# Kernel optimization log

Measured on AMD Instinct MI355X. Metric: run time of the kernel, lower is better.

Reference implementation:

```python
import jax, jax.numpy as jnp
import numpy as np
import math

B, S, HID = 16, 512, 768
NUM_LABELS = 9
NUM_HEADS = 4
HEAD_DIM = HID // NUM_HEADS
MAX_REL = 5
B_PERSON = 1
I_PERSON = 2
LN_EPS = 1e-5


def setup_inputs() -> dict:
    key = jax.random.key(0)
    ks = jax.random.split(key, 16)
    w = lambda k, shp: jax.random.normal(k, shp, dtype=jnp.float32) * 0.02
    return {
        "sequence_output": jax.random.normal(ks[0], (B, S, HID), dtype=jnp.float32),
        "Wq": w(ks[1], (HID, HID)), "bq": jnp.zeros((HID,), jnp.float32),
        "Wk": w(ks[2], (HID, HID)), "bk": jnp.zeros((HID,), jnp.float32),
        "Wv": w(ks[3], (HID, HID)), "bv": jnp.zeros((HID,), jnp.float32),
        "Wo": w(ks[4], (HID, HID)), "bo": jnp.zeros((HID,), jnp.float32),
        "ln_g": jnp.ones((HID,), jnp.float32), "ln_b": jnp.zeros((HID,), jnp.float32),
        "Ws": w(ks[5], (HID, NUM_LABELS)), "bs": jnp.zeros((NUM_LABELS,), jnp.float32),
        "entity_bias": w(ks[6], (NUM_LABELS,)),
    }


def _heads(x):
    # [B,S,HID] -> [B,H,S,D]
    return x.reshape(B, S, NUM_HEADS, HEAD_DIM).transpose(0, 2, 1, 3)


def reference(sequence_output, Wq, bq, Wk, bk, Wv, bv, Wo, bo, ln_g, ln_b, Ws, bs, entity_bias):
    x = sequence_output
    q = _heads(x @ Wq + bq)
    k = _heads(x @ Wk + bk)
    v = _heads(x @ Wv + bv)

    scores = jnp.einsum("bhqd,bhkd->bhqk", q, k)
    # relative position bias: exp(-0.1 * clamp(|i-j|, 0, MAX_REL)), broadcast over b,h
    idx = jnp.arange(S, dtype=jnp.float32)
    dist = jnp.abs(idx[None, :] - idx[:, None])  # [S,S]
    rel_bias = jnp.exp(-0.1 * jnp.clip(dist, 0.0, float(MAX_REL)))
    dist_mask = -0.1 * dist
    scores = (scores + rel_bias) / math.sqrt(HEAD_DIM) + dist_mask
    probs = jax.nn.softmax(scores, axis=-1)  # dropout is identity in eval

    ctx = jnp.einsum("bhqk,bhkd->bhqd", probs, v)
    ctx = ctx.transpose(0, 2, 1, 3).reshape(B, S, HID)
    out = ctx @ Wo + bo

    h = x + out
    mu = jnp.mean(h, axis=-1, keepdims=True)
    var = jnp.mean(jnp.square(h - mu), axis=-1, keepdims=True)
    h = (h - mu) * jax.lax.rsqrt(var + LN_EPS) * ln_g + ln_b

    span_logits = h @ Ws + bs  # [B,S,L]
    # vectorized entity-bias post-process: the torch loop adds entity_bias[I_PERSON]
    # TWICE to final_logits[:, j, I_PERSON] whenever argmax(span_logits[:, j-1]) == B_PERSON
    prev_is_b = jnp.argmax(span_logits[:, :-1], axis=-1) == B_PERSON  # [B,S-1]
    bump = jnp.where(prev_is_b, 2.0 * entity_bias[I_PERSON], 0.0)
    final_logits = span_logits.at[:, 1:, I_PERSON].add(bump)
    return final_logits
```

## Files before the change

kernel.cpp:

```cpp
#include <hip/hip_runtime.h>
#include <math.h>

#define SEQ 512
#define HID 768
#define NBATCH 16
#define ROWS 8192
#define INV_SQRT_D 0.07216878364870323f

typedef short s8v __attribute__((ext_vector_type(8)));
typedef _Float16 h8v __attribute__((ext_vector_type(8)));
typedef float f4v __attribute__((ext_vector_type(4)));
typedef unsigned short u16;

__device__ __forceinline__ u16 f2h(float f) {
  _Float16 h = (_Float16)f;
  return __builtin_bit_cast(u16, h);
}

template <int KSTEPS>
__device__ __forceinline__ void mm_core128(
    const u16* __restrict__ A, const int lda,
    const u16* __restrict__ B, const int ldb,
    u16* lds, f4v (&acc)[4][4])
{
  const int tid = threadIdx.x;
  const int w = tid >> 6, ln = tid & 63;
  const u16* src = (w >> 1) ? B : A;
  const int ld = (w >> 1) ? ldb : lda;
  const int half = w & 1;
  const int srow = ln >> 2;
  const int csw  = ((ln & 3) - (ln >> 3)) & 3;
  const int ml = ln & 15, quad = ln >> 4;
  const int fo2 = ((quad + ((ln >> 1) & 3)) & 3) * 8;
  const int wr = (w >> 1) * 64, wc = (w & 1) * 64;

  const u16* gp[4];
  int lpo[4];
#pragma unroll
  for (int t = 0; t < 4; ++t) {
    const int row = half * 64 + t * 16 + srow;
    gp[t]  = src + (size_t)row * ld + csw * 8;
    lpo[t] = (w >> 1) * 4096 + half * 2048 + t * 512 + ln * 8;
  }
  s8v c[8];
#pragma unroll
  for (int t = 0; t < 4; ++t) {
    c[t]     = *(const s8v*)gp[t];
    c[4 + t] = *(const s8v*)(gp[t] + 32);
  }

  for (int kp = 0; kp < KSTEPS / 2; ++kp) {
    __syncthreads();
#pragma unroll
    for (int t = 0; t < 4; ++t) {
      *(s8v*)&lds[lpo[t]]        = c[t];
      *(s8v*)&lds[8192 + lpo[t]] = c[4 + t];
    }
    __syncthreads();
    if (kp + 1 < KSTEPS / 2) {
      const int k0 = (kp + 1) * 64;
#pragma unroll
      for (int t = 0; t < 4; ++t) {
        c[t]     = *(const s8v*)(gp[t] + k0);
        c[4 + t] = *(const s8v*)(gp[t] + k0 + 32);
      }
    }
#pragma unroll
    for (int sub = 0; sub < 2; ++sub) {
      const int so = sub * 8192;
      h8v a[4], b[4];
#pragma unroll
      for (int i = 0; i < 4; ++i)
        a[i] = *(const h8v*)&lds[so + (wr + i * 16 + ml) * 32 + fo2];
#pragma unroll
      for (int j = 0; j < 4; ++j)
        b[j] = *(const h8v*)&lds[so + 4096 + (wc + j * 16 + ml) * 32 + fo2];
#pragma unroll
      for (int i = 0; i < 4; ++i)
#pragma unroll
        for (int j = 0; j < 4; ++j)
          acc[i][j] = __builtin_amdgcn_mfma_f32_16x16x32_f16(a[i], b[j], acc[i][j], 0, 0, 0);
    }
  }
}

__global__ __launch_bounds__(256) void splitx(const float* __restrict__ x,
                                              u16* __restrict__ xh)
{
  const int i = blockIdx.x * 256 + threadIdx.x;
  const float4 v = ((const float4*)x)[i];
  ((ushort4*)xh)[i] = make_ushort4(f2h(v.x), f2h(v.y), f2h(v.z), f2h(v.w));
}

__global__ __launch_bounds__(256) void wsplit(
    const float* __restrict__ Wq, const float* __restrict__ Wk,
    const float* __restrict__ Wv, const float* __restrict__ Wo,
    u16* __restrict__ WTh)
{
  __shared__ float t[32][33];
  const int z = blockIdx.z;
  const float* W = (z == 0) ? Wq : (z == 1) ? Wk : (z == 2) ? Wv : Wo;
  const int n0 = blockIdx.x * 32, k0 = blockIdx.y * 32;
  const int tx = threadIdx.x & 31, ty = threadIdx.x >> 5;
#pragma unroll
  for (int i = 0; i < 4; ++i)
    t[ty + 8 * i][tx] = W[(size_t)(k0 + ty + 8 * i) * HID + n0 + tx];
  __syncthreads();
#pragma unroll
  for (int i = 0; i < 4; ++i) {
    const float v = t[tx][ty + 8 * i];
    const size_t idx = (size_t)z * HID * HID + (size_t)(n0 + ty + 8 * i) * HID + k0 + tx;
    WTh[idx] = f2h(v);
  }
}

__global__ __launch_bounds__(256, 3) void qkv_mm(
    const u16* __restrict__ xh, const u16* __restrict__ WTh,
    const float* __restrict__ bq, const float* __restrict__ bk, const float* __restrict__ bv,
    u16* __restrict__ qh, u16* __restrict__ kh, u16* __restrict__ vtmp16)
{
  __shared__ u16 lds[16384];
  const int id = blockIdx.x;
  const int xcd = id & 7;
  const int s = id >> 3;
  const int bx = s % 6;
  const int yl = (s / 6) & 7;
  const int z  = s / 48;
  const int bm = (yl * 8 + xcd) * 128;
  const int bn = bx * 128;
  const size_t wtoff = (size_t)z * HID * HID + (size_t)bn * HID;
  f4v acc[4][4];
#pragma unroll
  for (int i = 0; i < 4; ++i)
#pragma unroll
    for (int j = 0; j < 4; ++j) acc[i][j] = (f4v)0.f;
  mm_core128<24>(xh + (size_t)bm * HID, HID, WTh + wtoff, HID, lds, acc);
  const int tid = threadIdx.x, w = tid >> 6, ln = tid & 63;
  const int ml = ln & 15, quad = ln >> 4;
  const int wr = (w >> 1) * 64, wc = (w & 1) * 64;
  const float* bias = (z == 0) ? bq : (z == 1) ? bk : bv;
#pragma unroll
  for (int i = 0; i < 4; ++i)
#pragma unroll
    for (int j = 0; j < 4; ++j) {
      const int gcol = bn + wc + j * 16 + ml;
      const float bv_ = bias[gcol];
#pragma unroll
      for (int r = 0; r < 4; ++r) {
        const int grow = bm + wr + i * 16 + quad * 4 + r;
        const float v = acc[i][j][r] + bv_;
        const size_t idx = (size_t)grow * HID + gcol;
        if (z == 2)      vtmp16[idx] = f2h(v);
        else if (z == 0) qh[idx] = f2h(v);
        else             kh[idx] = f2h(v);
      }
    }
}

__global__ __launch_bounds__(256) void vtrans(const u16* __restrict__ vtmp16,
                                              u16* __restrict__ vTh)
{
  __shared__ u16 t[32][33];
  const int b = blockIdx.z, n0 = blockIdx.x * 32, c0 = blockIdx.y * 32;
  const int tx = threadIdx.x & 31, ty = threadIdx.x >> 5;
  const u16* src = vtmp16 + (size_t)b * SEQ * HID;
#pragma unroll
  for (int i = 0; i < 4; ++i)
    t[ty + 8 * i][tx] = src[(size_t)(c0 + ty + 8 * i) * HID + n0 + tx];
  __syncthreads();
#pragma unroll
  for (int i = 0; i < 4; ++i) {
    const size_t idx = (size_t)b * HID * SEQ + (size_t)(n0 + ty + 8 * i) * SEQ + c0 + tx;
    vTh[idx] = t[tx][ty + 8 * i];
  }
}

__global__ __launch_bounds__(256, 2) void attn_fused(
    const u16* __restrict__ qh, const u16* __restrict__ kh,
    const u16* __restrict__ vTh, u16* __restrict__ ch)
{
  __shared__ u16 lds[28928];
  __shared__ float gtab[1024];
  __shared__ float red[4][32];
  const int f = blockIdx.x;
  const int xcd = f & 7, s = f >> 3;
  const int z = xcd * 8 + (s >> 4);
  const int bm = (s & 15) * 32;
  const int b = z >> 2, hh = z & 3;
  const int tid = threadIdx.x, w = tid >> 6, ln = tid & 63;
  const int ml = ln & 15, quad = ln >> 4;

  for (int t = tid; t < 1023; t += 256) {
    const float fd = fabsf((float)(t - 511));
    gtab[t] = INV_SQRT_D * __expf(-0.1f * fminf(fd, 5.0f)) - 0.1f * fd;
  }

  const u16* qbase = qh + (size_t)(b * SEQ + bm) * HID + hh * 192;
  const u16* kbase = kh + (size_t)b * SEQ * HID + hh * 192;
  const u16* vbase = vTh + (size_t)b * HID * SEQ + (size_t)(hh * 192) * SEQ;

  h8v qf[2][6];
#pragma unroll
  for (int i = 0; i < 2; ++i)
#pragma unroll
    for (int ks = 0; ks < 6; ++ks)
      qf[i][ks] = *(const h8v*)(qbase + (size_t)(i * 16 + ml) * HID + ks * 32 + quad * 8);

  int koff[6], kldso[6], voff[6], vldso[6];
#pragma unroll
  for (int c = 0; c < 6; ++c) {
    const int cc = c * 256 + tid;
    const int krow = cc / 24, kcol = cc % 24;
    koff[c]  = krow * HID + kcol * 8;
    kldso[c] = krow * 200 + kcol * 8;
    const int vrow = cc >> 3, vcol = cc & 7;
    voff[c]  = vrow * SEQ + vcol * 8;
    vldso[c] = 12800 + vrow * 72 + vcol * 8;
  }
  s8v kc[6], vc[6];
#pragma unroll
  for (int c = 0; c < 6; ++c) {
    kc[c] = *(const s8v*)(kbase + koff[c]);
    vc[c] = *(const s8v*)(vbase + voff[c]);
  }

  f4v acc2[2][3];
#pragma unroll
  for (int i = 0; i < 2; ++i)
#pragma unroll
    for (int jj = 0; jj < 3; ++jj) acc2[i][jj] = (f4v)0.f;
  float rsum[2][4];
#pragma unroll
  for (int i = 0; i < 2; ++i)
#pragma unroll
    for (int r = 0; r < 4; ++r) rsum[i][r] = 0.f;

  for (int j = 0; j < 8; ++j) {
    __syncthreads();
#pragma unroll
    for (int c = 0; c < 6; ++c) {
      *(s8v*)&lds[kldso[c]] = kc[c];
      *(s8v*)&lds[vldso[c]] = vc[c];
    }
    __syncthreads();
    if (j < 7) {
      const int ko = (j + 1) * 64;
#pragma unroll
      for (int c = 0; c < 6; ++c) {
        kc[c] = *(const s8v*)(kbase + (size_t)ko * HID + koff[c]);
        vc[c] = *(const s8v*)(vbase + ko + voff[c]);
      }
    }
    f4v sacc[2];
    sacc[0] = (f4v)0.f; sacc[1] = (f4v)0.f;
    __builtin_amdgcn_s_setprio(1);
#pragma unroll
    for (int ks = 0; ks < 6; ++ks) {
      const h8v kf = *(const h8v*)&lds[(w * 16 + ml) * 200 + ks * 32 + quad * 8];
      sacc[0] = __builtin_amdgcn_mfma_f32_16x16x32_f16(qf[0][ks], kf, sacc[0], 0, 0, 0);
      sacc[1] = __builtin_amdgcn_mfma_f32_16x16x32_f16(qf[1][ks], kf, sacc[1], 0, 0, 0);
    }
    __builtin_amdgcn_s_setprio(0);
    const int scolg = j * 64 + w * 16 + ml;
#pragma unroll
    for (int i = 0; i < 2; ++i)
#pragma unroll
      for (int r = 0; r < 4; ++r) {
        const int lrow = i * 16 + quad * 4 + r;
        const float g = gtab[bm + lrow - scolg + 511];
        const float p = __expf(fmaf(sacc[i][r], INV_SQRT_D, g));
        rsum[i][r] += p;
        lds[26624 + lrow * 72 + w * 16 + ml] = f2h(p);
      }
    __syncthreads();
    __builtin_amdgcn_s_setprio(1);
#pragma unroll
    for (int ks = 0; ks < 2; ++ks) {
      h8v pf[2], vf[3];
#pragma unroll
      for (int i = 0; i < 2; ++i)
        pf[i] = *(const h8v*)&lds[26624 + (i * 16 + ml) * 72 + ks * 32 + quad * 8];
#pragma unroll
      for (int jj = 0; jj < 3; ++jj)
        vf[jj] = *(const h8v*)&lds[12800 + (w * 48 + jj * 16 + ml) * 72 + ks * 32 + quad * 8];
#pragma unroll
      for (int i = 0; i < 2; ++i)
#pragma unroll
        for (int jj = 0; jj < 3; ++jj)
          acc2[i][jj] = __builtin_amdgcn_mfma_f32_16x16x32_f16(pf[i], vf[jj], acc2[i][jj], 0, 0, 0);
    }
    __builtin_amdgcn_s_setprio(0);
  }

#pragma unroll
  for (int i = 0; i < 2; ++i)
#pragma unroll
    for (int r = 0; r < 4; ++r) {
      float t = rsum[i][r];
#pragma unroll
      for (int o = 1; o < 16; o <<= 1) t += __shfl_xor(t, o, 64);
      rsum[i][r] = t;
    }
  if (ml == 0) {
#pragma unroll
    for (int i = 0; i < 2; ++i)
#pragma unroll
      for (int r = 0; r < 4; ++r) red[w][i * 16 + quad * 4 + r] = rsum[i][r];
  }
  __syncthreads();

#pragma unroll
  for (int i = 0; i < 2; ++i)
#pragma unroll
    for (int r = 0; r < 4; ++r) {
      const int R = i * 16 + quad * 4 + r;
      const float is = 1.0f / (red[0][R] + red[1][R] + red[2][R] + red[3][R]);
      const int m = bm + R;
#pragma unroll
      for (int jj = 0; jj < 3; ++jj) {
        const int gcol = hh * 192 + w * 48 + jj * 16 + ml;
        ch[(size_t)(b * SEQ + m) * HID + gcol] = f2h(acc2[i][jj][r] * is);
      }
    }
}

__global__ __launch_bounds__(256, 3) void proj_mm(
    const u16* __restrict__ ch, const u16* __restrict__ WTh,
    const float* __restrict__ bo, const float* __restrict__ x, float* __restrict__ h)
{
  __shared__ u16 lds[16384];
  const int id = blockIdx.x;
  const int xcd = id & 7;
  const int s = id >> 3;
  const int bx = s % 6;
  const int yl = s / 6;
  const int bm = (yl * 8 + xcd) * 128;
  const int bn = bx * 128;
  const size_t wtoff = (size_t)3 * HID * HID + (size_t)bn * HID;
  f4v acc[4][4];
#pragma unroll
  for (int i = 0; i < 4; ++i)
#pragma unroll
    for (int j = 0; j < 4; ++j) acc[i][j] = (f4v)0.f;
  mm_core128<24>(ch + (size_t)bm * HID, HID, WTh + wtoff, HID, lds, acc);
  const int tid = threadIdx.x, w = tid >> 6, ln = tid & 63;
  const int ml = ln & 15, quad = ln >> 4;
  const int wr = (w >> 1) * 64, wc = (w & 1) * 64;
#pragma unroll
  for (int i = 0; i < 4; ++i)
#pragma unroll
    for (int j = 0; j < 4; ++j) {
      const int gcol = bn + wc + j * 16 + ml;
      const float bv_ = bo[gcol];
#pragma unroll
      for (int r = 0; r < 4; ++r) {
        const int grow = bm + wr + i * 16 + quad * 4 + r;
        const size_t idx = (size_t)grow * HID + gcol;
        h[idx] = acc[i][j][r] + bv_ + x[idx];
      }
    }
}

__global__ __launch_bounds__(256) void ln_logits_kernel(
    const float* __restrict__ h, const float* __restrict__ g,
    const float* __restrict__ bta, const float* __restrict__ Ws,
    const float* __restrict__ bsv, float* __restrict__ span)
{
  const int row = blockIdx.x;
  const int tid = threadIdx.x;
  const float* hr = h + (size_t)row * HID;
  const float x0 = hr[tid], x1 = hr[tid + 256], x2 = hr[tid + 512];
  float s = x0 + x1 + x2;
  float sq = x0 * x0 + x1 * x1 + x2 * x2;
#pragma unroll
  for (int o = 32; o > 0; o >>= 1) { s += __shfl_down(s, o, 64); sq += __shfl_down(sq, o, 64); }
  __shared__ float red[8];
  __shared__ float smu, srs;
  const int wid = tid >> 6, lid = tid & 63;
  if (lid == 0) { red[wid] = s; red[4 + wid] = sq; }
  __syncthreads();
  if (tid == 0) {
    const float ts = red[0] + red[1] + red[2] + red[3];
    const float tq = red[4] + red[5] + red[6] + red[7];
    const float mu = ts / 768.0f;
    const float var = tq / 768.0f - mu * mu;
    smu = mu; srs = rsqrtf(var + 1e-5f);
  }
  __syncthreads();
  const float mu = smu, rs = srs;
  const float n0 = (x0 - mu) * rs * g[tid] + bta[tid];
  const float n1 = (x1 - mu) * rs * g[tid + 256] + bta[tid + 256];
  const float n2 = (x2 - mu) * rs * g[tid + 512] + bta[tid + 512];
  float pl[9];
#pragma unroll
  for (int l = 0; l < 9; ++l)
    pl[l] = n0 * Ws[(size_t)tid * 9 + l]
          + n1 * Ws[(size_t)(tid + 256) * 9 + l]
          + n2 * Ws[(size_t)(tid + 512) * 9 + l];
#pragma unroll
  for (int l = 0; l < 9; ++l)
#pragma unroll
    for (int o = 32; o > 0; o >>= 1) pl[l] += __shfl_down(pl[l], o, 64);
  __shared__ float lred[4][9];
  if (lid == 0) {
#pragma unroll
    for (int l = 0; l < 9; ++l) lred[wid][l] = pl[l];
  }
  __syncthreads();
  if (tid < 9) {
    span[(size_t)row * 9 + tid] =
        lred[0][tid] + lred[1][tid] + lred[2][tid] + lred[3][tid] + bsv[tid];
  }
}

__global__ __launch_bounds__(256) void bump_kernel(
    const float* __restrict__ span, const float* __restrict__ eb, float* __restrict__ out)
{
  const int idx = blockIdx.x * 256 + threadIdx.x;
  if (idx >= ROWS) return;
  const int j = idx & (SEQ - 1);
  const float* sl = span + (size_t)idx * 9;
  float v[9];
#pragma unroll
  for (int l = 0; l < 9; ++l) v[l] = sl[l];
  if (j >= 1) {
    const float* sp = sl - 9;
    float m = sp[0]; int am = 0;
#pragma unroll
    for (int l = 1; l < 9; ++l) { const float t = sp[l]; if (t > m) { m = t; am = l; } }
    if (am == 1) v[2] += 2.0f * eb[2];
  }
#pragma unroll
  for (int l = 0; l < 9; ++l) out[(size_t)idx * 9 + l] = v[l];
}

extern "C" void kernel_launch(void* const* d_in, const int* in_sizes, int n_in,
                              void* d_out, int out_size, void* d_ws, size_t ws_size,
                              hipStream_t stream)
{
  (void)in_sizes; (void)n_in; (void)out_size; (void)ws_size;
  const float* x   = (const float*)d_in[0];
  const float* Wq  = (const float*)d_in[1];
  const float* bq  = (const float*)d_in[2];
  const float* Wk  = (const float*)d_in[3];
  const float* bk  = (const float*)d_in[4];
  const float* Wv  = (const float*)d_in[5];
  const float* bv  = (const float*)d_in[6];
  const float* Wo  = (const float*)d_in[7];
  const float* bo  = (const float*)d_in[8];
  const float* lng = (const float*)d_in[9];
  const float* lnb = (const float*)d_in[10];
  const float* Ws  = (const float*)d_in[11];
  const float* bs  = (const float*)d_in[12];
  const float* eb  = (const float*)d_in[13];
  float* out = (float*)d_out;

  char* ws = (char*)d_ws;
  u16* xh  = (u16*)(ws + 0);
  u16* vTh = xh;
  u16* WTh = (u16*)(ws + 25165824);
  u16* qh  = (u16*)(ws + 34603008);
  u16* kh  = (u16*)(ws + 59768832);
  u16* vtmp16 = (u16*)(ws + 84934656);
  float* hb = (float*)(ws + 84934656);
  float* spanb = (float*)(ws + 152043520);
  u16* ctxh = qh;

  splitx<<<dim3(1572864 / 256), 256, 0, stream>>>(x, xh);
  wsplit<<<dim3(24, 24, 4), 256, 0, stream>>>(Wq, Wk, Wv, Wo, WTh);
  qkv_mm<<<dim3(1152), 256, 0, stream>>>(xh, WTh, bq, bk, bv, qh, kh, vtmp16);
  vtrans<<<dim3(24, 16, 16), 256, 0, stream>>>(vtmp16, vTh);
  attn_fused<<<dim3(1024), 256, 0, stream>>>(qh, kh, vTh, ctxh);
  proj_mm<<<dim3(384), 256, 0, stream>>>(ctxh, WTh, bo, x, hb);
  ln_logits_kernel<<<dim3(ROWS), 256, 0, stream>>>(hb, lng, lnb, Ws, bs, spanb);
  bump_kernel<<<dim3(ROWS / 256), 256, 0, stream>>>(spanb, eb, out);
}
```

Baseline: 228.3 us.

## Fuse V transpose into QKV epilogue and load GEMM tiles directly into LDS

```diff
diff --git a/kernel.cpp b/kernel.cpp
--- a/kernel.cpp
+++ b/kernel.cpp
@@ -15,6 +15,12 @@
 __device__ __forceinline__ u16 f2h(float f) {
   _Float16 h = (_Float16)f;
   return __builtin_bit_cast(u16, h);
+}
+
+__device__ __forceinline__ void llds16(const u16* g, u16* l) {
+  __builtin_amdgcn_global_load_lds(
+      (const __attribute__((address_space(1))) void*)g,
+      (__attribute__((address_space(3))) void*)l, 16, 0, 0);
 }
 
 template <int KSTEPS>
@@ -30,41 +36,28 @@
   const int half = w & 1;
   const int srow = ln >> 2;
   const int csw  = ((ln & 3) - (ln >> 3)) & 3;
-  const int ml = ln & 15, quad = ln >> 4;
-  const int fo2 = ((quad + ((ln >> 1) & 3)) & 3) * 8;
+  const int ml = ln & 15;
+  const int fo2 = (((ln >> 4) + ((ln >> 1) & 3)) & 3) * 8;
   const int wr = (w >> 1) * 64, wc = (w & 1) * 64;
 
   const u16* gp[4];
-  int lpo[4];
+  u16* lp[4];
 #pragma unroll
   for (int t = 0; t < 4; ++t) {
     const int row = half * 64 + t * 16 + srow;
-    gp[t]  = src + (size_t)row * ld + csw * 8;
-    lpo[t] = (w >> 1) * 4096 + half * 2048 + t * 512 + ln * 8;
-  }
-  s8v c[8];
-#pragma unroll
-  for (int t = 0; t < 4; ++t) {
-    c[t]     = *(const s8v*)gp[t];
-    c[4 + t] = *(const s8v*)(gp[t] + 32);
+    gp[t] = src + (size_t)row * ld + csw * 8;
+    lp[t] = lds + (w >> 1) * 4096 + half * 2048 + t * 512;
   }
 
   for (int kp = 0; kp < KSTEPS / 2; ++kp) {
+    const int k0 = kp * 64;
     __syncthreads();
 #pragma unroll
     for (int t = 0; t < 4; ++t) {
-      *(s8v*)&lds[lpo[t]]        = c[t];
-      *(s8v*)&lds[8192 + lpo[t]] = c[4 + t];
+      llds16(gp[t] + k0,      lp[t]);
+      llds16(gp[t] + k0 + 32, lp[t] + 8192);
     }
     __syncthreads();
-    if (kp + 1 < KSTEPS / 2) {
-      const int k0 = (kp + 1) * 64;
-#pragma unroll
-      for (int t = 0; t < 4; ++t) {
-        c[t]     = *(const s8v*)(gp[t] + k0);
-        c[4 + t] = *(const s8v*)(gp[t] + k0 + 32);
-      }
-    }
 #pragma unroll
     for (int sub = 0; sub < 2; ++sub) {
       const int so = sub * 8192;
@@ -117,7 +110,7 @@
 __global__ __launch_bounds__(256, 3) void qkv_mm(
     const u16* __restrict__ xh, const u16* __restrict__ WTh,
     const float* __restrict__ bq, const float* __restrict__ bk, const float* __restrict__ bv,
-    u16* __restrict__ qh, u16* __restrict__ kh, u16* __restrict__ vtmp16)
+    u16* __restrict__ qh, u16* __restrict__ kh, u16* __restrict__ vTh)
 {
   __shared__ u16 lds[16384];
   const int id = blockIdx.x;
@@ -138,40 +131,35 @@
   const int tid = threadIdx.x, w = tid >> 6, ln = tid & 63;
   const int ml = ln & 15, quad = ln >> 4;
   const int wr = (w >> 1) * 64, wc = (w & 1) * 64;
-  const float* bias = (z == 0) ? bq : (z == 1) ? bk : bv;
-#pragma unroll
-  for (int i = 0; i < 4; ++i)
-#pragma unroll
-    for (int j = 0; j < 4; ++j) {
-      const int gcol = bn + wc + j * 16 + ml;
-      const float bv_ = bias[gcol];
-#pragma unroll
-      for (int r = 0; r < 4; ++r) {
-        const int grow = bm + wr + i * 16 + quad * 4 + r;
-        const float v = acc[i][j][r] + bv_;
-        const size_t idx = (size_t)grow * HID + gcol;
-        if (z == 2)      vtmp16[idx] = f2h(v);
-        else if (z == 0) qh[idx] = f2h(v);
-        else             kh[idx] = f2h(v);
-      }
-    }
-}
-
-__global__ __launch_bounds__(256) void vtrans(const u16* __restrict__ vtmp16,
-                                              u16* __restrict__ vTh)
-{
-  __shared__ u16 t[32][33];
-  const int b = blockIdx.z, n0 = blockIdx.x * 32, c0 = blockIdx.y * 32;
-  const int tx = threadIdx.x & 31, ty = threadIdx.x >> 5;
-  const u16* src = vtmp16 + (size_t)b * SEQ * HID;
-#pragma unroll
-  for (int i = 0; i < 4; ++i)
-    t[ty + 8 * i][tx] = src[(size_t)(c0 + ty + 8 * i) * HID + n0 + tx];
-  __syncthreads();
-#pragma unroll
-  for (int i = 0; i < 4; ++i) {
-    const size_t idx = (size_t)b * HID * SEQ + (size_t)(n0 + ty + 8 * i) * SEQ + c0 + tx;
-    vTh[idx] = t[tx][ty + 8 * i];
+  if (z == 2) {
+    u16* vb = vTh + (size_t)(bm >> 9) * HID * SEQ;
+    const int spbase = (bm & 511) + wr + quad * 4;
+#pragma unroll
+    for (int i = 0; i < 4; ++i)
+#pragma unroll
+      for (int j = 0; j < 4; ++j) {
+        const int gcol = bn + wc + j * 16 + ml;
+        const float bv_ = bv[gcol];
+        const ushort4 pk = make_ushort4(
+            f2h(acc[i][j][0] + bv_), f2h(acc[i][j][1] + bv_),
+            f2h(acc[i][j][2] + bv_), f2h(acc[i][j][3] + bv_));
+        *(ushort4*)&vb[(size_t)gcol * SEQ + spbase + i * 16] = pk;
+      }
+  } else {
+    const float* bias = (z == 0) ? bq : bk;
+    u16* dst = (z == 0) ? qh : kh;
+#pragma unroll
+    for (int i = 0; i < 4; ++i)
+#pragma unroll
+      for (int j = 0; j < 4; ++j) {
+        const int gcol = bn + wc + j * 16 + ml;
+        const float bv_ = bias[gcol];
+#pragma unroll
+        for (int r = 0; r < 4; ++r) {
+          const int grow = bm + wr + i * 16 + quad * 4 + r;
+          dst[(size_t)grow * HID + gcol] = f2h(acc[i][j][r] + bv_);
+        }
+      }
   }
 }
 
@@ -457,19 +445,17 @@
 
   char* ws = (char*)d_ws;
   u16* xh  = (u16*)(ws + 0);
-  u16* vTh = xh;
   u16* WTh = (u16*)(ws + 25165824);
   u16* qh  = (u16*)(ws + 34603008);
   u16* kh  = (u16*)(ws + 59768832);
-  u16* vtmp16 = (u16*)(ws + 84934656);
+  u16* vTh = (u16*)(ws + 84934656);
   float* hb = (float*)(ws + 84934656);
   float* spanb = (float*)(ws + 152043520);
   u16* ctxh = qh;
 
   splitx<<<dim3(1572864 / 256), 256, 0, stream>>>(x, xh);
   wsplit<<<dim3(24, 24, 4), 256, 0, stream>>>(Wq, Wk, Wv, Wo, WTh);
-  qkv_mm<<<dim3(1152), 256, 0, stream>>>(xh, WTh, bq, bk, bv, qh, kh, vtmp16);
-  vtrans<<<dim3(24, 16, 16), 256, 0, stream>>>(vtmp16, vTh);
+  qkv_mm<<<dim3(1152), 256, 0, stream>>>(xh, WTh, bq, bk, bv, qh, kh, vTh);
   attn_fused<<<dim3(1024), 256, 0, stream>>>(qh, kh, vTh, ctxh);
   proj_mm<<<dim3(384), 256, 0, stream>>>(ctxh, WTh, bo, x, hb);
   ln_logits_kernel<<<dim3(ROWS), 256, 0, stream>>>(hb, lng, lnb, Ws, bs, spanb);
```

New measurement: 226.8 us. About the same (-0.6%).
